# Kernel tuning notes

Measured on AMD Instinct MI355X. Metric: run time of the kernel, lower is better.

## Reference

```python
import jax, jax.numpy as jnp
import numpy as np

NH, NKV, HD = 32, 8, 128      # query heads, kv heads, head dim
B, S, H = 4, 1024, 4096       # batch, per-seq tokens (prefill, no history), hidden
BLOCK = 64                    # paged KV-cache block size
BPS = S // BLOCK              # blocks per sequence


def rotate_half(x):
    x1, x2 = jnp.split(x, 2, axis=-1)
    return jnp.concatenate([-x2, x1], axis=-1)


def setup_inputs() -> dict:
    key = jax.random.key(0)
    ks = jax.random.split(key, 5)
    hidden_states = jax.random.normal(ks[0], (B * S, H), jnp.float32)
    Wq = jax.random.normal(ks[1], (H, NH * HD), jnp.float32) * 0.02
    Wk = jax.random.normal(ks[2], (H, NKV * HD), jnp.float32) * 0.02
    Wv = jax.random.normal(ks[3], (H, NKV * HD), jnp.float32) * 0.02
    Wo = jax.random.normal(ks[4], (NH * HD, H), jnp.float32) * 0.02
    # standard llama rope inverse frequencies
    inv_freq = 1.0 / (10000.0 ** (jnp.arange(0, HD, 2, dtype=jnp.float32) / HD))
    # empty paged KV cache: [num_blocks, block, n_kv_heads, head_dim]
    k_cache = jnp.zeros((B * BPS, BLOCK, NKV, HD), jnp.float32)
    v_cache = jnp.zeros((B * BPS, BLOCK, NKV, HD), jnp.float32)
    # per-token positions (prefill, history=0): 0..S-1 for each sequence
    position_ids_1d = jnp.tile(jnp.arange(S, dtype=jnp.int32), B)
    # block table: which cache block holds each logical block of each sequence
    block_offsets = jnp.arange(B * BPS, dtype=jnp.int32).reshape(B, BPS)
    return dict(hidden_states=hidden_states, Wq=Wq, Wk=Wk, Wv=Wv, Wo=Wo,
                inv_freq=inv_freq, k_cache=k_cache, v_cache=v_cache,
                position_ids_1d=position_ids_1d, block_offsets=block_offsets)


def reference(hidden_states, Wq, Wk, Wv, Wo, inv_freq, k_cache, v_cache,
              position_ids_1d, block_offsets):
    # qkv projections (contiguous-batching: tokens flattened)
    q = (hidden_states @ Wq).reshape(-1, NH, HD)
    k = (hidden_states @ Wk).reshape(-1, NKV, HD)
    v = (hidden_states @ Wv).reshape(-1, NKV, HD)

    # fused rotary: cos/sin from inv_freq at per-token 1d positions
    freqs = position_ids_1d.astype(jnp.float32)[:, None] * inv_freq[None, :]  # [T, HD/2]
    emb = jnp.concatenate([freqs, freqs], axis=-1)                            # [T, HD]
    cos = jnp.cos(emb)[:, None, :]
    sin = jnp.sin(emb)[:, None, :]
    q = q * cos + rotate_half(q) * sin
    k = k * cos + rotate_half(k) * sin

    # fill_kv_cache: scatter rotated K / raw V into paged cache via block_offsets
    flat_offsets = block_offsets.reshape(-1)
    k_blk = k.reshape(B * BPS, BLOCK, NKV, HD)
    v_blk = v.reshape(B * BPS, BLOCK, NKV, HD)
    k_cache = k_cache.at[flat_offsets].set(k_blk)
    v_cache = v_cache.at[flat_offsets].set(v_blk)

    # paged_attention_fwd: gather K/V blocks back via block table
    kk = k_cache[block_offsets].reshape(B, BPS * BLOCK, NKV, HD)  # [B, Skv, NKV, HD]
    vv = v_cache[block_offsets].reshape(B, BPS * BLOCK, NKV, HD)
    groups = NH // NKV
    kk = jnp.repeat(kk, groups, axis=2)  # repeat_kv -> [B, Skv, NH, HD]
    vv = jnp.repeat(vv, groups, axis=2)

    qb = q.reshape(B, S, NH, HD)
    scale = 1.0 / jnp.sqrt(jnp.float32(HD))
    scores = jnp.einsum('bqhd,bkhd->bhqk', qb, kk) * scale  # [B, NH, S, Skv]
    causal = jnp.arange(S)[:, None] >= jnp.arange(BPS * BLOCK)[None, :]
    scores = jnp.where(causal[None, None], scores, jnp.float32(-1e30))
    probs = jax.nn.softmax(scores, axis=-1)
    attn = jnp.einsum('bhqk,bkhd->bqhd', probs, vv).reshape(B * S, NH * HD)
    return attn @ Wo
```

## Files before the change

### kernel.cpp

```cpp
#include <hip/hip_runtime.h>
#include <cstdint>
#include <cstddef>


typedef unsigned short u16;
typedef __bf16 bf16x8 __attribute__((ext_vector_type(8)));
typedef float  f32x4  __attribute__((ext_vector_type(4)));

#define SEQ 1024
#define QKV_COLS 6144
#define NHEAD 32
#define NKVH 8
#define HDIM 128

__device__ __forceinline__ u16 f2bf(float f) {
  union { float f; uint32_t u; } v; v.f = f;
  return (u16)((v.u + 0x7fffu + ((v.u >> 16) & 1u)) >> 16);
}
__device__ __forceinline__ float bf2f(u16 x) {
  union { uint32_t u; float f; } v; v.u = ((uint32_t)x) << 16;
  return v.f;
}

typedef __attribute__((address_space(1))) const uint32_t g_u32;
typedef __attribute__((address_space(3))) uint32_t l_u32;
__device__ __forceinline__ void async_copy16(const u16* g, u16* lds_base) {
  __builtin_amdgcn_global_load_lds((g_u32*)g, (l_u32*)lds_base, 16, 0, 0);
}

__global__ void cast_f32_bf16(const float* __restrict__ in, u16* __restrict__ out, int n) {
  int i = (blockIdx.x * 256 + threadIdx.x) * 4;
  if (i >= n) return;
  float4 v = *(const float4*)&in[i];
  uint2 pk;
  pk.x = (uint32_t)f2bf(v.x) | ((uint32_t)f2bf(v.y) << 16);
  pk.y = (uint32_t)f2bf(v.z) | ((uint32_t)f2bf(v.w) << 16);
  *(uint2*)&out[i] = pk;
}

__global__ void transpose_f32_bf16(const float* __restrict__ in, u16* __restrict__ out,
                                   int R, int C) {
  __shared__ float tile[32][33];
  int c0 = blockIdx.x * 32, r0 = blockIdx.y * 32;
  int tx = threadIdx.x, ty = threadIdx.y;
  tile[ty][tx] = in[(size_t)(r0 + ty) * C + c0 + tx];
  __syncthreads();
  out[(size_t)(c0 + ty) * R + r0 + tx] = f2bf(tile[tx][ty]);
}

template <int MODE>
__global__ __launch_bounds__(512, 2) void gemm_bt(const u16* __restrict__ A,
                                                  const u16* __restrict__ Bt,
                                                  void* __restrict__ Cv,
                                                  u16* __restrict__ Vt,
                                                  int M, int N, int K, int ldc,
                                                  int nbx) {
  __shared__ __align__(16) u16 smem[4][2][256 * 32];

  const int tid = threadIdx.x;
  const int lane = tid & 63, wave = tid >> 6;
  const int l15 = lane & 15, qd = lane >> 4;
  const int wm = wave >> 2, wn = wave & 3;

  const int nwg = gridDim.x;
  const int bid = (int)blockIdx.x;
  const int swz = (bid & 7) * (nwg >> 3) + (bid >> 3);
  const int bx = swz % nbx, by = swz / nbx;
  const int row0 = by * 256, col0 = bx * 256;

  const int sl = (qd ^ (l15 & 3) ^ (l15 >> 2)) * 8;

  int soff[2], cb[2];
#pragma unroll
  for (int call = 0; call < 2; ++call) {
    const int c = call * 512 + tid;
    const int r = c >> 2, j = c & 3;
    const int src = j ^ (r & 3) ^ ((r >> 2) & 3);
    soff[call] = r * K + src * 8;
    cb[call] = (call * 512 + wave * 64) * 8;
  }

  const u16* Ab = A + (size_t)row0 * K;
  const u16* Bb = Bt + (size_t)col0 * K;
  const int NT = K >> 5;

  f32x4 acc[8][4] = {};

#pragma unroll
  for (int tt = 0; tt < 3; ++tt) {
#pragma unroll
    for (int call = 0; call < 2; ++call)
      async_copy16(&Ab[tt * 32 + soff[call]], &smem[tt][0][cb[call]]);
#pragma unroll
    for (int call = 0; call < 2; ++call)
      async_copy16(&Bb[tt * 32 + soff[call]], &smem[tt][1][cb[call]]);
  }
  asm volatile("s_waitcnt vmcnt(8)" ::: "memory");
  __builtin_amdgcn_s_barrier();

  for (int t = 0; t < NT; ++t) {
    const int bsel = t & 3, ssel = (t + 3) & 3;
    const u16* As = &smem[bsel][0][0];
    const u16* Bs = &smem[bsel][1][0];
    const bool do_stage = (t + 3) < NT;
    const int knext = (t + 3) * 32;

    bf16x8 af[4], bfr[4];
#pragma unroll
    for (int i = 0; i < 4; ++i) {
      af[i]  = *(const bf16x8*)&As[(wm * 128 + i * 16 + l15) * 32 + sl];
      bfr[i] = *(const bf16x8*)&Bs[(wn * 64 + i * 16 + l15) * 32 + sl];
    }
    if (do_stage) {
#pragma unroll
      for (int call = 0; call < 2; ++call)
        async_copy16(&Ab[knext + soff[call]], &smem[ssel][0][cb[call]]);
    }
    __builtin_amdgcn_s_barrier();
    asm volatile("s_waitcnt lgkmcnt(0)" ::: "memory");
    __builtin_amdgcn_sched_barrier(0);
    __builtin_amdgcn_s_setprio(1);
#pragma unroll
    for (int mi = 0; mi < 4; ++mi)
#pragma unroll
      for (int ni = 0; ni < 4; ++ni)
        acc[mi][ni] = __builtin_amdgcn_mfma_f32_16x16x32_bf16(af[mi], bfr[ni], acc[mi][ni], 0, 0, 0);
    __builtin_amdgcn_s_setprio(0);
    __builtin_amdgcn_sched_barrier(0);
    __builtin_amdgcn_s_barrier();

#pragma unroll
    for (int i = 0; i < 4; ++i)
      af[i] = *(const bf16x8*)&As[(wm * 128 + (4 + i) * 16 + l15) * 32 + sl];
    if (do_stage) {
#pragma unroll
      for (int call = 0; call < 2; ++call)
        async_copy16(&Bb[knext + soff[call]], &smem[ssel][1][cb[call]]);
    }
    __builtin_amdgcn_s_barrier();
    asm volatile("s_waitcnt lgkmcnt(0)" ::: "memory");
    __builtin_amdgcn_sched_barrier(0);
    __builtin_amdgcn_s_setprio(1);
#pragma unroll
    for (int mi = 0; mi < 4; ++mi)
#pragma unroll
      for (int ni = 0; ni < 4; ++ni)
        acc[4 + mi][ni] = __builtin_amdgcn_mfma_f32_16x16x32_bf16(af[mi], bfr[ni], acc[4 + mi][ni], 0, 0, 0);
    __builtin_amdgcn_s_setprio(0);
    __builtin_amdgcn_sched_barrier(0);

    if (t < NT - 1) {
      if (t < NT - 3)       asm volatile("s_waitcnt vmcnt(8)" ::: "memory");
      else if (t == NT - 3) asm volatile("s_waitcnt vmcnt(4)" ::: "memory");
      else                  asm volatile("s_waitcnt vmcnt(0)" ::: "memory");
      __builtin_amdgcn_s_barrier();
    }
  }

  if (MODE == 0 && col0 >= 5120) {
#pragma unroll
    for (int mi = 0; mi < 8; ++mi)
#pragma unroll
      for (int ni = 0; ni < 4; ++ni) {
        const int col = col0 + wn * 64 + ni * 16 + l15;
        const int dcol = col - 5120, kvh = dcol >> 7, d = dcol & 127;
        const int row = row0 + wm * 128 + mi * 16 + qd * 4;
        const int bb = row >> 10, p = row & 1023;
        ushort4 pk;
        pk.x = f2bf(acc[mi][ni][0]); pk.y = f2bf(acc[mi][ni][1]);
        pk.z = f2bf(acc[mi][ni][2]); pk.w = f2bf(acc[mi][ni][3]);
        *(ushort4*)&Vt[(((size_t)(bb * 8 + kvh) * 128) + d) * 1024 + p] = pk;
      }
    return;
  }
#pragma unroll
  for (int mi = 0; mi < 8; ++mi)
#pragma unroll
    for (int ni = 0; ni < 4; ++ni)
#pragma unroll
      for (int r = 0; r < 4; ++r) {
        int row = row0 + wm * 128 + mi * 16 + qd * 4 + r;
        int col = col0 + wn * 64 + ni * 16 + l15;
        float v = acc[mi][ni][r];
        if (MODE == 1) ((float*)Cv)[(size_t)row * ldc + col] = v;
        else           ((u16*)Cv)[(size_t)row * ldc + col] = f2bf(v);
      }
}

__global__ void rope_kernel(u16* __restrict__ qkv, const float* __restrict__ inv_freq,
                            const int* __restrict__ pos) {
  int idx = blockIdx.x * 256 + threadIdx.x;
  int t = idx / 2560;
  int r = idx - t * 2560;
  int hh = r >> 6, i = r & 63;
  float f = (float)pos[t] * inv_freq[i];
  float s, c;
  sincosf(f, &s, &c);
  size_t base = (size_t)t * QKV_COLS + hh * HDIM + i;
  float x1 = bf2f(qkv[base]), x2 = bf2f(qkv[base + 64]);
  qkv[base]      = f2bf(x1 * c - x2 * s);
  qkv[base + 64] = f2bf(x2 * c + x1 * s);
}

__global__ __launch_bounds__(512, 4) void attn_kernel(const u16* __restrict__ qkv,
                                                      const u16* __restrict__ vt,
                                                      u16* __restrict__ ao) {
  __shared__ __align__(16) u16 Ks[64 * 136];
  __shared__ __align__(16) u16 Vts[128 * 68];
  __shared__ __align__(16) u16 Ps[8][16 * 68];

  const int tid = threadIdx.x;
  const int lane = tid & 63, wave = tid >> 6;
  const int l15 = lane & 15, qd = lane >> 4;
  const int qt = blockIdx.x, h = blockIdx.y, b = blockIdx.z;
  const int q0 = qt * 128;
  const int kvh = h >> 2;
  const float scale = 0.08838834764831845f;

  bf16x8 qf[4];
  {
    const size_t qrow = (size_t)(b * SEQ + q0 + wave * 16 + l15) * QKV_COLS + h * HDIM;
#pragma unroll
    for (int s = 0; s < 4; ++s) qf[s] = *(const bf16x8*)&qkv[qrow + s * 32 + qd * 8];
  }

  f32x4 o[8] = {};
  float mrow[4] = {-__builtin_inff(), -__builtin_inff(), -__builtin_inff(), -__builtin_inff()};
  float lrow[4] = {0.f, 0.f, 0.f, 0.f};

  const int nkt = qt * 2 + 2;
  const size_t vbase0 = ((size_t)(b * NKVH + kvh) * HDIM) * SEQ;
  for (int kt = 0; kt < nkt; ++kt) {
    const int kv0 = kt * 64;
#pragma unroll
    for (int rnd = 0; rnd < 2; ++rnd) {
      int c = tid + rnd * 512;
      int kv = c >> 4, dc = (c & 15) * 8;
      *(uint4*)&Ks[kv * 136 + dc] =
          *(const uint4*)&qkv[(size_t)(b * SEQ + kv0 + kv) * QKV_COLS + 4096 + kvh * HDIM + dc];
    }
#pragma unroll
    for (int rnd = 0; rnd < 2; ++rnd) {
      int c = tid + rnd * 512;
      int d = c >> 3, kc = (c & 7) * 8;
      *(uint4*)&Vts[d * 68 + kc] = *(const uint4*)&vt[vbase0 + (size_t)d * SEQ + kv0 + kc];
    }
    __syncthreads();

    f32x4 st[4] = {};
#pragma unroll
    for (int t = 0; t < 4; ++t)
#pragma unroll
      for (int s = 0; s < 4; ++s) {
        bf16x8 kf = *(const bf16x8*)&Ks[(t * 16 + l15) * 136 + s * 32 + qd * 8];
        st[t] = __builtin_amdgcn_mfma_f32_16x16x32_bf16(qf[s], kf, st[t], 0, 0, 0);
      }

    float al[4];
#pragma unroll
    for (int r = 0; r < 4; ++r) {
      const int qpos = q0 + wave * 16 + qd * 4 + r;
      float sc[4];
#pragma unroll
      for (int t = 0; t < 4; ++t) {
        sc[t] = st[t][r] * scale;
        if (kv0 + t * 16 + l15 > qpos) sc[t] = -1e30f;
      }
      float mt = fmaxf(fmaxf(sc[0], sc[1]), fmaxf(sc[2], sc[3]));
      mt = fmaxf(mt, __shfl_xor(mt, 8));
      mt = fmaxf(mt, __shfl_xor(mt, 4));
      mt = fmaxf(mt, __shfl_xor(mt, 2));
      mt = fmaxf(mt, __shfl_xor(mt, 1));
      const float mn = fmaxf(mrow[r], mt);
      al[r] = __expf(mrow[r] - mn);
      float p[4], rs = 0.f;
#pragma unroll
      for (int t = 0; t < 4; ++t) { p[t] = __expf(sc[t] - mn); rs += p[t]; }
      rs += __shfl_xor(rs, 8);
      rs += __shfl_xor(rs, 4);
      rs += __shfl_xor(rs, 2);
      rs += __shfl_xor(rs, 1);
      lrow[r] = lrow[r] * al[r] + rs;
      mrow[r] = mn;
#pragma unroll
      for (int t = 0; t < 4; ++t)
        Ps[wave][(qd * 4 + r) * 68 + t * 16 + l15] = f2bf(p[t]);
    }
    asm volatile("s_waitcnt lgkmcnt(0)" ::: "memory");

    {
      const int srcl = (l15 >> 2) * 16;
      float a0 = __shfl(al[0], srcl), a1 = __shfl(al[1], srcl);
      float a2 = __shfl(al[2], srcl), a3 = __shfl(al[3], srcl);
      const int rr = l15 & 3;
      float aq = (rr & 2) ? ((rr & 1) ? a3 : a2) : ((rr & 1) ? a1 : a0);
#pragma unroll
      for (int dt = 0; dt < 8; ++dt) o[dt] *= aq;
    }
    {
      const bf16x8 pf0 = *(const bf16x8*)&Ps[wave][l15 * 68 + qd * 8];
      const bf16x8 pf1 = *(const bf16x8*)&Ps[wave][l15 * 68 + 32 + qd * 8];
#pragma unroll
      for (int dt = 0; dt < 8; ++dt) {
        const bf16x8 vf0 = *(const bf16x8*)&Vts[(dt * 16 + l15) * 68 + qd * 8];
        const bf16x8 vf1 = *(const bf16x8*)&Vts[(dt * 16 + l15) * 68 + 32 + qd * 8];
        o[dt] = __builtin_amdgcn_mfma_f32_16x16x32_bf16(vf0, pf0, o[dt], 0, 0, 0);
        o[dt] = __builtin_amdgcn_mfma_f32_16x16x32_bf16(vf1, pf1, o[dt], 0, 0, 0);
      }
    }
    __syncthreads();
  }

  {
    const int srcl = (l15 >> 2) * 16;
    float l0 = __shfl(lrow[0], srcl), l1 = __shfl(lrow[1], srcl);
    float l2 = __shfl(lrow[2], srcl), l3 = __shfl(lrow[3], srcl);
    const int rr = l15 & 3;
    float lq = (rr & 2) ? ((rr & 1) ? l3 : l2) : ((rr & 1) ? l1 : l0);
    const float inv = 1.0f / lq;
    const size_t obase = (size_t)(b * SEQ + q0 + wave * 16 + l15) * (NHEAD * HDIM) + h * HDIM;
#pragma unroll
    for (int dt = 0; dt < 8; ++dt) {
      ushort4 pk;
      pk.x = f2bf(o[dt][0] * inv); pk.y = f2bf(o[dt][1] * inv);
      pk.z = f2bf(o[dt][2] * inv); pk.w = f2bf(o[dt][3] * inv);
      *(ushort4*)&ao[obase + dt * 16 + qd * 4] = pk;
    }
  }
}

extern "C" void kernel_launch(void* const* d_in, const int* in_sizes, int n_in,
                              void* d_out, int out_size, void* d_ws, size_t ws_size,
                              hipStream_t stream) {
  const float* X    = (const float*)d_in[0];
  const float* Wq   = (const float*)d_in[1];
  const float* Wk   = (const float*)d_in[2];
  const float* Wv   = (const float*)d_in[3];
  const float* Wo   = (const float*)d_in[4];
  const float* invf = (const float*)d_in[5];
  const int*   pos  = (const int*)d_in[8];
  float* out = (float*)d_out;

  char* ws = (char*)d_ws;
  u16* Xbf   = (u16*)(ws + 0);
  u16* Wqkvt = (u16*)(ws + 33554432);
  u16* Wot   = (u16*)(ws + 83886080);
  u16* QKV   = (u16*)(ws + 117440512);
  u16* Vt    = (u16*)(ws + 167772160);
  u16* AO    = Xbf;

  dim3 tb32(32, 32);
  cast_f32_bf16<<<16384, 256, 0, stream>>>(X, Xbf, 16777216);
  transpose_f32_bf16<<<dim3(128, 128), tb32, 0, stream>>>(Wq, Wqkvt, 4096, 4096);
  transpose_f32_bf16<<<dim3(32, 128),  tb32, 0, stream>>>(Wk, Wqkvt + (size_t)4096 * 4096, 4096, 1024);
  transpose_f32_bf16<<<dim3(32, 128),  tb32, 0, stream>>>(Wv, Wqkvt + (size_t)5120 * 4096, 4096, 1024);
  transpose_f32_bf16<<<dim3(128, 128), tb32, 0, stream>>>(Wo, Wot, 4096, 4096);

  gemm_bt<0><<<dim3(24 * 16), 512, 0, stream>>>(Xbf, Wqkvt, QKV, Vt, 4096, 6144, 4096, 6144, 24);
  rope_kernel<<<40960, 256, 0, stream>>>(QKV, invf, pos);
  attn_kernel<<<dim3(8, 32, 4), 512, 0, stream>>>(QKV, Vt, AO);
  gemm_bt<1><<<dim3(16 * 16), 512, 0, stream>>>(AO, Wot, out, Vt, 4096, 4096, 4096, 4096, 16);
}
```

Before: 865.7 us.

## Prefetch next k-tile fragments into registers and cut GEMM loop barriers

Restructures the GEMM main loop to software-pipeline LDS fragment loads. The first A/B fragments of the next k-tile are loaded during the current tile's second MFMA phase and carried across iterations in registers. Two of the three per-iteration barriers and the explicit lgkmcnt waits are removed, and the vmcnt waits are tightened, so global staging now waits one tile earlier. This lowers barrier and LDS-latency stalls between MFMA bursts, at the cost of more registers and a subtler ordering argument for LDS buffer reuse.

```diff
diff --git a/kernel.cpp b/kernel.cpp
--- a/kernel.cpp
+++ b/kernel.cpp
@@ -95,66 +95,71 @@
     for (int call = 0; call < 2; ++call)
       async_copy16(&Bb[tt * 32 + soff[call]], &smem[tt][1][cb[call]]);
   }
-  asm volatile("s_waitcnt vmcnt(8)" ::: "memory");
+  asm volatile("s_waitcnt vmcnt(4)" ::: "memory");
   __builtin_amdgcn_s_barrier();
-
+  asm volatile("" ::: "memory");
+
+  bf16x8 a0[4], b0[4];
+#pragma unroll
+  for (int i = 0; i < 4; ++i) {
+    a0[i] = *(const bf16x8*)&smem[0][0][(wm * 128 + i * 16 + l15) * 32 + sl];
+    b0[i] = *(const bf16x8*)&smem[0][1][(wn * 64 + i * 16 + l15) * 32 + sl];
+  }
+
+#pragma unroll 2
   for (int t = 0; t < NT; ++t) {
-    const int bsel = t & 3, ssel = (t + 3) & 3;
-    const u16* As = &smem[bsel][0][0];
-    const u16* Bs = &smem[bsel][1][0];
+    const int bsel = t & 3, nsel = (t + 1) & 3, ssel = (t + 3) & 3;
     const bool do_stage = (t + 3) < NT;
     const int knext = (t + 3) * 32;
 
-    bf16x8 af[4], bfr[4];
-#pragma unroll
-    for (int i = 0; i < 4; ++i) {
-      af[i]  = *(const bf16x8*)&As[(wm * 128 + i * 16 + l15) * 32 + sl];
-      bfr[i] = *(const bf16x8*)&Bs[(wn * 64 + i * 16 + l15) * 32 + sl];
-    }
+    bf16x8 a1[4];
+#pragma unroll
+    for (int i = 0; i < 4; ++i)
+      a1[i] = *(const bf16x8*)&smem[bsel][0][(wm * 128 + 64 + i * 16 + l15) * 32 + sl];
     if (do_stage) {
 #pragma unroll
       for (int call = 0; call < 2; ++call)
         async_copy16(&Ab[knext + soff[call]], &smem[ssel][0][cb[call]]);
     }
-    __builtin_amdgcn_s_barrier();
-    asm volatile("s_waitcnt lgkmcnt(0)" ::: "memory");
     __builtin_amdgcn_sched_barrier(0);
     __builtin_amdgcn_s_setprio(1);
 #pragma unroll
     for (int mi = 0; mi < 4; ++mi)
 #pragma unroll
       for (int ni = 0; ni < 4; ++ni)
-        acc[mi][ni] = __builtin_amdgcn_mfma_f32_16x16x32_bf16(af[mi], bfr[ni], acc[mi][ni], 0, 0, 0);
+        acc[mi][ni] = __builtin_amdgcn_mfma_f32_16x16x32_bf16(a0[mi], b0[ni], acc[mi][ni], 0, 0, 0);
     __builtin_amdgcn_s_setprio(0);
-    __builtin_amdgcn_sched_barrier(0);
-    __builtin_amdgcn_s_barrier();
-
-#pragma unroll
-    for (int i = 0; i < 4; ++i)
-      af[i] = *(const bf16x8*)&As[(wm * 128 + (4 + i) * 16 + l15) * 32 + sl];
+
+    bf16x8 a2[4], b2[4];
+    if (t + 1 < NT) {
+#pragma unroll
+      for (int i = 0; i < 4; ++i) {
+        a2[i] = *(const bf16x8*)&smem[nsel][0][(wm * 128 + i * 16 + l15) * 32 + sl];
+        b2[i] = *(const bf16x8*)&smem[nsel][1][(wn * 64 + i * 16 + l15) * 32 + sl];
+      }
+    }
     if (do_stage) {
 #pragma unroll
       for (int call = 0; call < 2; ++call)
         async_copy16(&Bb[knext + soff[call]], &smem[ssel][1][cb[call]]);
     }
-    __builtin_amdgcn_s_barrier();
-    asm volatile("s_waitcnt lgkmcnt(0)" ::: "memory");
     __builtin_amdgcn_sched_barrier(0);
     __builtin_amdgcn_s_setprio(1);
 #pragma unroll
     for (int mi = 0; mi < 4; ++mi)
 #pragma unroll
       for (int ni = 0; ni < 4; ++ni)
-        acc[4 + mi][ni] = __builtin_amdgcn_mfma_f32_16x16x32_bf16(af[mi], bfr[ni], acc[4 + mi][ni], 0, 0, 0);
+        acc[4 + mi][ni] = __builtin_amdgcn_mfma_f32_16x16x32_bf16(a1[mi], b0[ni], acc[4 + mi][ni], 0, 0, 0);
     __builtin_amdgcn_s_setprio(0);
-    __builtin_amdgcn_sched_barrier(0);
-
-    if (t < NT - 1) {
-      if (t < NT - 3)       asm volatile("s_waitcnt vmcnt(8)" ::: "memory");
-      else if (t == NT - 3) asm volatile("s_waitcnt vmcnt(4)" ::: "memory");
-      else                  asm volatile("s_waitcnt vmcnt(0)" ::: "memory");
+
+    if (t < NT - 2) {
+      if (t < NT - 3) asm volatile("s_waitcnt vmcnt(4)" ::: "memory");
+      else            asm volatile("s_waitcnt vmcnt(0)" ::: "memory");
       __builtin_amdgcn_s_barrier();
-    }
+      asm volatile("" ::: "memory");
+    }
+#pragma unroll
+    for (int i = 0; i < 4; ++i) { a0[i] = a2[i]; b0[i] = b2[i]; }
   }
 
   if (MODE == 0 && col0 >= 5120) {
```

Result: faster. 812.1 us (-6.2%).
